# Optimization experiments

Hardware: AMD Instinct MI355X
Metric: run time of the kernel (lower is better)

The kernel has to match this reference:

```python
import jax, jax.numpy as jnp
import numpy as np

N = 30000      # nodes
E = 480000     # edges
F = 128        # num_node_features (== C, required by LSTM-JK stacking of h_list incl. x)
C = 128        # graph_hidden_channels
K = 8          # kernel_size (num gaussians)
D = 2          # pseudo-coordinate dim
L = 4          # nlayers
H = (L * C) // 2   # PyG JK-LSTM hidden size = 256
NHID = 512
NOUT = 256
B = 1024       # number of graphs in batch
EPS = 1e-15


def setup_inputs() -> dict:
    key = jax.random.key(0)
    ks = jax.random.split(key, 24)
    s = 0.05
    inp = {}
    inp['x'] = jax.random.normal(ks[0], (N, F), jnp.float32)
    inp['edge_index'] = jax.random.randint(ks[1], (2, E), 0, N, dtype=jnp.int32)
    inp['edge_attr'] = jax.random.uniform(ks[2], (E, D), jnp.float32)
    inp['batch'] = jnp.sort(jax.random.randint(ks[3], (N,), 0, B, dtype=jnp.int32))
    # GMMConv params per layer (Cin == C for all layers since F == C)
    inp['g'] = jax.random.normal(ks[4], (L, F, K * C), jnp.float32) * s
    inp['root'] = jax.random.normal(ks[5], (L, F, C), jnp.float32) * s
    inp['bias'] = jnp.zeros((L, C), jnp.float32)
    inp['mu'] = jax.random.uniform(ks[6], (L, K, D), jnp.float32)
    inp['sigma'] = jax.random.uniform(ks[7], (L, K, D), jnp.float32) * 0.5 + 0.5
    inp['bn_gamma'] = jnp.ones((L, C), jnp.float32)
    inp['bn_beta'] = jnp.zeros((L, C), jnp.float32)
    # Bidirectional LSTM for JumpingKnowledge: dir 0 = fwd, dir 1 = bwd; gate order i,f,g,o
    inp['w_ih'] = jax.random.normal(ks[8], (2, 4 * H, C), jnp.float32) * s
    inp['w_hh'] = jax.random.normal(ks[9], (2, 4 * H, H), jnp.float32) * s
    inp['b_ih'] = jnp.zeros((2, 4 * H), jnp.float32)
    inp['b_hh'] = jnp.zeros((2, 4 * H), jnp.float32)
    inp['att_w'] = jax.random.normal(ks[10], (2 * H, 1), jnp.float32) * s
    inp['att_b'] = jnp.zeros((1,), jnp.float32)
    inp['p1_w'] = jax.random.normal(ks[11], (C, NHID), jnp.float32) * s
    inp['p1_b'] = jnp.zeros((NHID,), jnp.float32)
    inp['p2_w'] = jax.random.normal(ks[12], (NHID, NOUT), jnp.float32) * s
    inp['p2_b'] = jnp.zeros((NOUT,), jnp.float32)
    inp['ln_g'] = jnp.ones((NOUT,), jnp.float32)
    inp['ln_b'] = jnp.zeros((NOUT,), jnp.float32)
    return inp


def _lstm_dir(xs, w_ih, w_hh, b_ih, b_hh, reverse):
    # xs: [T, N, C] -> hidden states [T, N, H], aligned with input order
    def step(carry, xt):
        h, c = carry
        gates = xt @ w_ih.T + h @ w_hh.T + (b_ih + b_hh)
        i, f, g, o = jnp.split(gates, 4, axis=-1)
        c = jax.nn.sigmoid(f) * c + jax.nn.sigmoid(i) * jnp.tanh(g)
        h = jax.nn.sigmoid(o) * jnp.tanh(c)
        return (h, c), h
    h0 = jnp.zeros((xs.shape[1], w_hh.shape[1]), xs.dtype)
    _, hs = jax.lax.scan(step, (h0, h0), xs, reverse=reverse)
    return hs


def reference(x, edge_index, edge_attr, batch, g, root, bias, mu, sigma,
              bn_gamma, bn_beta, w_ih, w_hh, b_ih, b_hh, att_w, att_b,
              p1_w, p1_b, p2_w, p2_b, ln_g, ln_b):
    src, dst = edge_index[0], edge_index[1]
    deg = jnp.maximum(jax.ops.segment_sum(jnp.ones((E,), x.dtype), dst, num_segments=N), 1.0)[:, None]
    h = x
    h_list = [x]
    for i in range(L):
        # GMMConv: node-level transform then gaussian-weighted message passing (mean aggr)
        xg = (h @ g[i]).reshape(N, K, C)                     # [N, K, C]
        diff = edge_attr[:, None, :] - mu[i][None]           # [E, K, D]
        w = jnp.exp(jnp.sum(-0.5 * diff ** 2 / (EPS + sigma[i][None] ** 2), axis=-1))  # [E, K]
        msg = jnp.zeros((E, C), x.dtype)
        for k in range(K):                                   # small fixed K; avoids [E,K,C] gather
            msg = msg + w[:, k:k + 1] * xg[src, k, :]
        agg = jax.ops.segment_sum(msg, dst, num_segments=N) / deg
        h = agg + h @ root[i] + bias[i]
        # BatchNorm1d (training-mode batch statistics)
        mean = h.mean(0)
        var = h.var(0)
        h = (h - mean) / jnp.sqrt(var + 1e-5) * bn_gamma[i] + bn_beta[i]
        if i < L - 1:
            h = jax.nn.relu(h)
        # dropout is identity in eval mode
        h_list.append(h)
    # JumpingKnowledge, mode='lstm'
    xs = jnp.stack(h_list, axis=0)                           # [L+1, N, C]
    hf = _lstm_dir(xs, w_ih[0], w_hh[0], b_ih[0], b_hh[0], False)
    hb = _lstm_dir(xs, w_ih[1], w_hh[1], b_ih[1], b_hh[1], True)
    seq = jnp.concatenate([hf, hb], axis=-1)                 # [L+1, N, 2H]
    alpha = (seq @ att_w)[..., 0] + att_b[0]                 # [L+1, N]
    alpha = jax.nn.softmax(alpha, axis=0)
    node_rep = jnp.sum(alpha[..., None] * xs, axis=0)        # [N, C]
    # global_mean_pool
    cnt = jnp.maximum(jax.ops.segment_sum(jnp.ones((N,), x.dtype), batch, num_segments=B), 1.0)
    h_graph = jax.ops.segment_sum(node_rep, batch, num_segments=B) / cnt[:, None]
    z = jax.nn.relu(h_graph @ p1_w + p1_b)
    z = z @ p2_w + p2_b
    zm = z.mean(-1, keepdims=True)
    zv = z.var(-1, keepdims=True)
    return (z - zm) / jnp.sqrt(zv + 1e-5) * ln_g + ln_b
```

## Files before the change

kernel.cpp:

```cpp
#include <hip/hip_runtime.h>
#include <hip/hip_bf16.h>
#include <math.h>

#define N_    30000
#define E_    480000
#define C_    128
#define K_    8
#define L_    4
#define H_    256
#define NHID_ 512
#define NOUT_ 256
#define B_    1024
#define SCAN_B 30

typedef __attribute__((ext_vector_type(8))) short short8;
typedef __attribute__((ext_vector_type(4))) float floatx4;
typedef __hip_bfloat16 bf16;

static inline size_t align256(size_t x){ return (x + 255) & ~(size_t)255; }

__device__ __forceinline__ void gload_lds16(const void* g, void* l){
  __builtin_amdgcn_global_load_lds((const __attribute__((address_space(1))) void*)g,
                                   (__attribute__((address_space(3))) void*)l, 16, 0, 0);
}
__device__ __forceinline__ float bf2f(short s){
  union { unsigned u; float f; } x; x.u = ((unsigned)(unsigned short)s) << 16; return x.f;
}

__global__ void hist_k(const int* __restrict__ dst, int* __restrict__ cnt){
  int e = blockIdx.x*256 + threadIdx.x;
  if (e < E_) atomicAdd(&cnt[dst[e]], 1);
}

__global__ void scan1_k(const int* __restrict__ cnt, int* __restrict__ rowptr, int* __restrict__ btot){
  __shared__ int sh[1024];
  int i = blockIdx.x*1024 + (int)threadIdx.x;
  int v = (i < N_) ? cnt[i] : 0;
  sh[threadIdx.x] = v;
  __syncthreads();
  for (int o = 1; o < 1024; o <<= 1){
    int t = (threadIdx.x >= (unsigned)o) ? sh[threadIdx.x - o] : 0;
    __syncthreads();
    sh[threadIdx.x] += t;
    __syncthreads();
  }
  if (i < N_) rowptr[i] = sh[threadIdx.x] - v;
  if (threadIdx.x == 1023) btot[blockIdx.x] = sh[1023];
}
__global__ void scan2_k(const int* __restrict__ btot, int* __restrict__ boff){
  if (threadIdx.x == 0){
    int s = 0;
    for (int b = 0; b < SCAN_B; b++){ boff[b] = s; s += btot[b]; }
    boff[SCAN_B] = s;
  }
}
__global__ void scan3_k(int* __restrict__ rowptr, const int* __restrict__ boff){
  int i = blockIdx.x*1024 + (int)threadIdx.x;
  if (i < N_) rowptr[i] += boff[blockIdx.x];
  if (i == N_-1) rowptr[N_] = boff[SCAN_B];
}

__global__ void degf_k(const int* __restrict__ cnt, float* __restrict__ degf){
  int n = blockIdx.x*256 + threadIdx.x;
  if (n < N_) degf[n] = fmaxf((float)cnt[n], 1.0f);
}

__global__ void scatter_k(const int* __restrict__ src, const int* __restrict__ dst,
                          const int* __restrict__ rowptr, int* __restrict__ fill,
                          int* __restrict__ srcsort, int* __restrict__ edgepos){
  int e = blockIdx.x*256 + threadIdx.x;
  if (e >= E_) return;
  int d = dst[e];
  int pos = rowptr[d] + atomicAdd(&fill[d], 1);
  srcsort[pos] = src[e];
  edgepos[e] = pos;
}

__global__ void cast_k(const float* __restrict__ in, bf16* __restrict__ out, int n){
  int i = blockIdx.x*256 + threadIdx.x;
  if (i < n) out[i] = __float2bfloat16(in[i]);
}
__global__ void tcast_k(const float* __restrict__ in, bf16* __restrict__ out, int R, int Cc){
  const float* ip = in + (size_t)blockIdx.y*R*Cc;
  bf16* op = out + (size_t)blockIdx.y*R*Cc;
  int i = blockIdx.x*256 + threadIdx.x;
  if (i >= R*Cc) return;
  int c = i / R, r = i - c*R;
  op[i] = __float2bfloat16(ip[(size_t)r*Cc + c]);
}
__global__ void gtcast_k(const float* __restrict__ in, bf16* __restrict__ out){
  const float* ip = in + (size_t)blockIdx.y*C_*(K_*C_);
  bf16* op = out + (size_t)blockIdx.y*C_*(K_*C_);
  int i = blockIdx.x*256 + threadIdx.x;
  int co = i >> 10;
  int rem = i & 1023;
  int k = rem >> 7, c = rem & 127;
  op[i] = __float2bfloat16(ip[(size_t)c*(K_*C_) + k*C_ + co]);
}
__global__ void permcast_k(const float* __restrict__ in, bf16* __restrict__ out, int Kdim){
  const float* ip = in + (size_t)blockIdx.y*1024*Kdim;
  bf16* op = out + (size_t)blockIdx.y*1024*Kdim;
  int i = blockIdx.x*256 + threadIdx.x;
  if (i >= 1024*Kdim) return;
  int r = i / Kdim, k = i - r*Kdim;
  int gsel = r >> 8, j = r & 255;
  int rp = ((j >> 5) << 7) + gsel*32 + (j & 31);
  op[(size_t)rp*Kdim + k] = __float2bfloat16(ip[i]);
}
__global__ void permbias_k(const float* __restrict__ bih, const float* __restrict__ bhh,
                           float* __restrict__ bp){
  int i = blockIdx.x*256 + threadIdx.x;
  if (i >= 2048) return;
  int dir = i >> 10, r = i & 1023;
  int gsel = r >> 8, j = r & 255;
  int rp = ((j >> 5) << 7) + gsel*32 + (j & 31);
  bp[dir*1024 + rp] = bih[i] + bhh[i];
}

template<int OUTBF16, int STATS>
__global__ __launch_bounds__(256)
void gemm_bf16_k(const bf16* __restrict__ A1, const bf16* __restrict__ B1, int K1,
                 const bf16* __restrict__ A2, const bf16* __restrict__ B2, int K2,
                 const float* __restrict__ bias1, const float* __restrict__ bias2,
                 void* __restrict__ Cout, int M, int Nn, int relu,
                 float* __restrict__ stats)
{
  __shared__ short As[128*32];
  __shared__ short Bs[128*32];
  __shared__ float colstat[256];
  const int tid  = threadIdx.x;
  const int wave = tid >> 6, lane = tid & 63;
  const int m0 = blockIdx.y*128, n0 = blockIdx.x*128;
  const int wm = (wave >> 1)*64, wn = (wave & 1)*64;
  const int lrow = lane & 15, lk = lane >> 4;
  floatx4 acc[4][4] = {};
  if (STATS) colstat[tid] = 0.f;

  #pragma unroll
  for (int phase = 0; phase < 2; ++phase){
    const bf16* A = phase ? A2 : A1;
    const bf16* B = phase ? B2 : B1;
    const int   K = phase ? K2 : K1;
    if (A == nullptr) continue;
    for (int k0 = 0; k0 < K; k0 += 32){
      #pragma unroll
      for (int i = 0; i < 2; ++i){
        const int chunkbase = i*256 + wave*64;
        const int c   = chunkbase + lane;
        const int row = c >> 2, cc = (c & 3) << 3;
        int ar = m0 + row; if (ar >= M) ar = M - 1;
        gload_lds16(A + (size_t)ar*K + k0 + cc,        As + (size_t)chunkbase*8);
        gload_lds16(B + (size_t)(n0 + row)*K + k0 + cc, Bs + (size_t)chunkbase*8);
      }
      __syncthreads();
      short8 af[4], bfr[4];
      #pragma unroll
      for (int t = 0; t < 4; ++t){
        af[t]  = *(const short8*)&As[((size_t)(wm + t*16 + lrow))*32 + lk*8];
        bfr[t] = *(const short8*)&Bs[((size_t)(wn + t*16 + lrow))*32 + lk*8];
      }
      #pragma unroll
      for (int mt = 0; mt < 4; ++mt)
        #pragma unroll
        for (int nt = 0; nt < 4; ++nt)
          acc[mt][nt] = __builtin_amdgcn_mfma_f32_16x16x32_bf16(af[mt], bfr[nt], acc[mt][nt], 0, 0, 0);
      __syncthreads();
    }
  }

  float* outf = (float*)Cout;
  bf16*  outb = (bf16*)Cout;
  #pragma unroll
  for (int nt = 0; nt < 4; ++nt){
    const int col = n0 + wn + nt*16 + lrow;
    float bv = bias1 ? bias1[col] : 0.f;
    if (bias2) bv += bias2[col];
    float s = 0.f, s2 = 0.f;
    #pragma unroll
    for (int mt = 0; mt < 4; ++mt){
      #pragma unroll
      for (int r = 0; r < 4; ++r){
        const int row = m0 + wm + mt*16 + lk*4 + r;
        if (row >= M) continue;
        float v = acc[mt][nt][r] + bv;
        if (relu) v = fmaxf(v, 0.f);
        if (OUTBF16) outb[(size_t)row*Nn + col] = __float2bfloat16(v);
        else         outf[(size_t)row*Nn + col] = v;
        if (STATS){ s += v; s2 += v*v; }
      }
    }
    if (STATS){
      s  += __shfl_down(s, 16);  s  += __shfl_down(s, 32);
      s2 += __shfl_down(s2, 16); s2 += __shfl_down(s2, 32);
      if (lane < 16){
        atomicAdd(&colstat[wn + nt*16 + lane], s);
        atomicAdd(&colstat[128 + wn + nt*16 + lane], s2);
      }
    }
  }
  if (STATS){
    __syncthreads();
    if (tid < 128){
      atomicAdd(&stats[tid],       colstat[tid]);
      atomicAdd(&stats[128 + tid], colstat[128 + tid]);
    }
  }
}

__global__ __launch_bounds__(256)
void lstm_step_k(const bf16* __restrict__ A1, const bf16* __restrict__ B1,
                 const bf16* __restrict__ A2, const bf16* __restrict__ B2,
                 const float* __restrict__ bp,
                 bf16* __restrict__ hout, float* __restrict__ cst,
                 const float* __restrict__ attw, float* __restrict__ alpha,
                 int M)
{
  __shared__ short As[128*32];
  __shared__ short Bs[128*32];
  __shared__ short gt[128*136];
  const int tid  = threadIdx.x;
  const int wave = tid >> 6, lane = tid & 63;
  const int m0 = blockIdx.y*128, n0 = blockIdx.x*128;
  const int wm = (wave >> 1)*64, wn = (wave & 1)*64;
  const int lrow = lane & 15, lk = lane >> 4;
  floatx4 acc[4][4] = {};

  #pragma unroll
  for (int phase = 0; phase < 2; ++phase){
    const bf16* A = phase ? A2 : A1;
    const bf16* B = phase ? B2 : B1;
    const int   K = phase ? H_ : C_;
    if (A == nullptr) continue;
    for (int k0 = 0; k0 < K; k0 += 32){
      #pragma unroll
      for (int i = 0; i < 2; ++i){
        const int chunkbase = i*256 + wave*64;
        const int c   = chunkbase + lane;
        const int row = c >> 2, cc = (c & 3) << 3;
        int ar = m0 + row; if (ar >= M) ar = M - 1;
        gload_lds16(A + (size_t)ar*K + k0 + cc,        As + (size_t)chunkbase*8);
        gload_lds16(B + (size_t)(n0 + row)*K + k0 + cc, Bs + (size_t)chunkbase*8);
      }
      __syncthreads();
      short8 af[4], bfr[4];
      #pragma unroll
      for (int t = 0; t < 4; ++t){
        af[t]  = *(const short8*)&As[((size_t)(wm + t*16 + lrow))*32 + lk*8];
        bfr[t] = *(const short8*)&Bs[((size_t)(wn + t*16 + lrow))*32 + lk*8];
      }
      #pragma unroll
      for (int mt = 0; mt < 4; ++mt)
        #pragma unroll
        for (int nt = 0; nt < 4; ++nt)
          acc[mt][nt] = __builtin_amdgcn_mfma_f32_16x16x32_bf16(af[mt], bfr[nt], acc[mt][nt], 0, 0, 0);
      __syncthreads();
    }
  }

  #pragma unroll
  for (int nt = 0; nt < 4; ++nt){
    const int col = wn + nt*16 + lrow;
    const float bv = bp[n0 + col];
    #pragma unroll
    for (int mt = 0; mt < 4; ++mt){
      #pragma unroll
      for (int r = 0; r < 4; ++r){
        const int row = wm + mt*16 + lk*4 + r;
        bf16 q = __float2bfloat16(acc[mt][nt][r] + bv);
        gt[row*136 + col] = __builtin_bit_cast(short, q);
      }
    }
  }
  __syncthreads();

  const int row  = tid >> 1, half = tid & 1;
  const int grow = m0 + row;
  float att = 0.f;
  if (grow < M){
    const int chbase = half*16;
    const int jbase  = blockIdx.x*32 + chbase;
    const short8* gp = (const short8*)&gt[row*136 + chbase];
    short8 gv[4][2];
    #pragma unroll
    for (int gsel = 0; gsel < 4; ++gsel){
      gv[gsel][0] = gp[gsel*4];
      gv[gsel][1] = gp[gsel*4 + 1];
    }
    const size_t base = (size_t)grow*H_ + jbase;
    floatx4 cold[4];
    if (A2){
      #pragma unroll
      for (int q = 0; q < 4; ++q) cold[q] = ((const floatx4*)(cst + base))[q];
    } else {
      #pragma unroll
      for (int q = 0; q < 4; ++q) cold[q] = (floatx4){0.f,0.f,0.f,0.f};
    }
    floatx4 cnew[4];
    __hip_bfloat162 hb[8];
    #pragma unroll
    for (int i = 0; i < 16; ++i){
      float gi = bf2f(gv[0][i>>3][i&7]);
      float gf = bf2f(gv[1][i>>3][i&7]);
      float gg = bf2f(gv[2][i>>3][i&7]);
      float go = bf2f(gv[3][i>>3][i&7]);
      float co = cold[i>>2][i&3];
      float ig = 1.f/(1.f + expf(-gi));
      float fg = 1.f/(1.f + expf(-gf));
      float gtv = tanhf(gg);
      float og = 1.f/(1.f + expf(-go));
      float cv = fg*co + ig*gtv;
      float hv = og*tanhf(cv);
      cnew[i>>2][i&3] = cv;
      bf16 hq = __float2bfloat16(hv);
      if (i & 1) hb[i>>1].y = hq; else hb[i>>1].x = hq;
      att = fmaf(hv, attw[jbase + i], att);
    }
    #pragma unroll
    for (int q = 0; q < 4; ++q) ((floatx4*)(cst + base))[q] = cnew[q];
    float4* hp = (float4*)(hout + base);
    hp[0] = *(float4*)&hb[0];
    hp[1] = *(float4*)&hb[4];
  }
  att += __shfl_down(att, 1);
  if (grow < M && half == 0) atomicAdd(&alpha[grow], att);
}

__global__ void compute_w_k(const float* __restrict__ ea, const float* __restrict__ mu,
                            const float* __restrict__ sigma, const int* __restrict__ edgepos,
                            float* __restrict__ wsrt)
{
  int e = blockIdx.x*256 + threadIdx.x;
  if (e >= E_) return;
  float a0 = ea[2*e], a1 = ea[2*e+1];
  int pos = edgepos[e];
  float outv[8];
  #pragma unroll
  for (int k = 0; k < 8; k++){
    float d0 = a0 - mu[2*k],   d1 = a1 - mu[2*k+1];
    float s0 = sigma[2*k],     s1 = sigma[2*k+1];
    float t = -0.5f*(d0*d0/(1e-15f + s0*s0) + d1*d1/(1e-15f + s1*s1));
    outv[k] = expf(t);
  }
  float4* op = (float4*)(wsrt + (size_t)pos*8);
  op[0] = make_float4(outv[0], outv[1], outv[2], outv[3]);
  op[1] = make_float4(outv[4], outv[5], outv[6], outv[7]);
}

__global__ __launch_bounds__(256)
void aggregate_t_k(const bf16* __restrict__ h, const float* __restrict__ wsrt,
                   const int* __restrict__ rowptr, const int* __restrict__ srcsort,
                   const float* __restrict__ degf, bf16* __restrict__ t)
{
  int node = blockIdx.x*4 + (threadIdx.x >> 6);
  int lane = threadIdx.x & 63;
  if (node >= N_) return;
  int p0 = rowptr[node], p1 = rowptr[node+1];
  float ax[8] = {}, ay[8] = {};
  for (int p = p0; p < p1; p++){
    int s = srcsort[p];
    const float4 w03 = *(const float4*)(wsrt + (size_t)p*8);
    const float4 w47 = *(const float4*)(wsrt + (size_t)p*8 + 4);
    const float wk[8] = {w03.x,w03.y,w03.z,w03.w,w47.x,w47.y,w47.z,w47.w};
    float2 v = __bfloat1622float2(((const __hip_bfloat162*)(h + (size_t)s*C_))[lane]);
    #pragma unroll
    for (int k = 0; k < 8; k++){
      ax[k] = fmaf(wk[k], v.x, ax[k]);
      ay[k] = fmaf(wk[k], v.y, ay[k]);
    }
  }
  float inv = 1.0f / degf[node];
  __hip_bfloat162* tp = (__hip_bfloat162*)(t + (size_t)node*(K_*C_));
  #pragma unroll
  for (int k = 0; k < 8; k++){
    __hip_bfloat162 o; o.x = __float2bfloat16(ax[k]*inv); o.y = __float2bfloat16(ay[k]*inv);
    tp[k*64 + lane] = o;
  }
}

__global__ void bn_apply_k(const float* __restrict__ hpre, const float* __restrict__ stats,
                           const float* __restrict__ gamma, const float* __restrict__ beta,
                           bf16* __restrict__ outp, int relu)
{
  int i = blockIdx.x*256 + threadIdx.x;
  if (i >= N_*C_) return;
  int c = i & 127;
  float mean = stats[c] * (1.0f/N_);
  float var  = stats[c+128] * (1.0f/N_) - mean*mean;
  float rstd = rsqrtf(var + 1e-5f);
  float v = (hpre[i] - mean)*rstd*gamma[c] + beta[c];
  if (relu) v = fmaxf(v, 0.f);
  outp[i] = __float2bfloat16(v);
}

__global__ void jk_pool_k(const float* __restrict__ x, const bf16* __restrict__ hlist,
                          const float* __restrict__ alpha, const int* __restrict__ batch,
                          float* __restrict__ hgraph, float* __restrict__ gcnt)
{
  int n = blockIdx.x, c = threadIdx.x;
  float a[5]; float mx = -1e30f;
  #pragma unroll
  for (int t = 0; t < 5; t++){ a[t] = alpha[(size_t)t*N_ + n]; mx = fmaxf(mx, a[t]); }
  float ssum = 0.f;
  #pragma unroll
  for (int t = 0; t < 5; t++){ a[t] = expf(a[t] - mx); ssum += a[t]; }
  float inv = 1.0f/ssum;
  float val = a[0]*inv*x[(size_t)n*C_ + c];
  #pragma unroll
  for (int t = 1; t < 5; t++)
    val = fmaf(a[t]*inv, __bfloat162float(hlist[((size_t)(t-1)*N_ + n)*C_ + c]), val);
  int bg = batch[n];
  atomicAdd(&hgraph[(size_t)bg*C_ + c], val);
  if (c == 0) atomicAdd(&gcnt[bg], 1.0f);
}

__global__ void pool_div_k(const float* __restrict__ hg, const float* __restrict__ gcnt,
                           bf16* __restrict__ hgb){
  int i = blockIdx.x*256 + threadIdx.x;
  if (i < B_*C_) hgb[i] = __float2bfloat16(hg[i] / fmaxf(gcnt[i >> 7], 1.0f));
}

__global__ __launch_bounds__(256)
void layernorm_k(float* __restrict__ z, const float* __restrict__ g, const float* __restrict__ b){
  int row = blockIdx.x, j = threadIdx.x;
  float v = z[(size_t)row*NOUT_ + j];
  float s = v, s2 = v*v;
  #pragma unroll
  for (int o = 32; o; o >>= 1){ s += __shfl_down(s, o); s2 += __shfl_down(s2, o); }
  __shared__ float sh[8];
  int w = j >> 6;
  if ((j & 63) == 0){ sh[w] = s; sh[4+w] = s2; }
  __syncthreads();
  float st  = sh[0] + sh[1] + sh[2] + sh[3];
  float st2 = sh[4] + sh[5] + sh[6] + sh[7];
  float mean = st * (1.0f/NOUT_);
  float var  = st2 * (1.0f/NOUT_) - mean*mean;
  float rstd = rsqrtf(var + 1e-5f);
  z[(size_t)row*NOUT_ + j] = (v - mean)*rstd*g[j] + b[j];
}

extern "C" void kernel_launch(void* const* d_in, const int* in_sizes, int n_in,
                              void* d_out, int out_size, void* d_ws, size_t ws_size,
                              hipStream_t stream)
{
  (void)in_sizes; (void)n_in; (void)out_size; (void)ws_size;
  const float* x     = (const float*)d_in[0];
  const int*   eidx  = (const int*)  d_in[1];
  const float* eattr = (const float*)d_in[2];
  const int*   batch = (const int*)  d_in[3];
  const float* g     = (const float*)d_in[4];
  const float* root  = (const float*)d_in[5];
  const float* bias  = (const float*)d_in[6];
  const float* mu    = (const float*)d_in[7];
  const float* sigma = (const float*)d_in[8];
  const float* bng   = (const float*)d_in[9];
  const float* bnb   = (const float*)d_in[10];
  const float* w_ih  = (const float*)d_in[11];
  const float* w_hh  = (const float*)d_in[12];
  const float* b_ih  = (const float*)d_in[13];
  const float* b_hh  = (const float*)d_in[14];
  const float* attw  = (const float*)d_in[15];
  const float* p1w   = (const float*)d_in[17];
  const float* p1b   = (const float*)d_in[18];
  const float* p2w   = (const float*)d_in[19];
  const float* p2b   = (const float*)d_in[20];
  const float* lng   = (const float*)d_in[21];
  const float* lnb   = (const float*)d_in[22];
  float* outp = (float*)d_out;

  const int* src = eidx;
  const int* dst = eidx + E_;

  size_t off = 0;
  char* wsb = (char*)d_ws;
  auto carve = [&](size_t bytes)->void*{ void* p = wsb + off; off = align256(off + bytes); return p; };
  bf16*  hlist  = (bf16*) carve((size_t)L_*N_*C_*2);
  void*  big    =         carve((size_t)N_*(K_*C_)*2);
  void*  uni    =         carve((size_t)2*N_*H_*2 + (size_t)N_*H_*4 + 256);
  bf16*  xb     = (bf16*) carve((size_t)N_*C_*2);
  float* alpha  = (float*)carve((size_t)(L_+1)*N_*4);
  float* hgraph = (float*)carve((size_t)B_*C_*4);
  bf16*  hgb    = (bf16*) carve((size_t)B_*C_*2);
  float* gcnt   = (float*)carve((size_t)B_*4);
  bf16*  z1b    = (bf16*) carve((size_t)B_*NHID_*2);
  float* bnstats= (float*)carve((size_t)L_*2*C_*4);
  float* degf   = (float*)carve((size_t)N_*4);
  int* cnt      = (int*)  carve((size_t)N_*4);
  int* rowptr   = (int*)  carve((size_t)(N_+1)*4);
  int* fill     = (int*)  carve((size_t)N_*4);
  int* srcsort  = (int*)  carve((size_t)E_*4);
  int* edgepos  = (int*)  carve((size_t)E_*4);
  int* btot     = (int*)  carve((size_t)(SCAN_B+1)*4);
  int* boff     = (int*)  carve((size_t)(SCAN_B+1)*4);
  bf16* gGT   = (bf16*)carve((size_t)L_*C_*(K_*C_)*2);
  bf16* rootT = (bf16*)carve((size_t)L_*C_*C_*2);
  bf16* wihp  = (bf16*)carve((size_t)2*4*H_*C_*2);
  bf16* whhp  = (bf16*)carve((size_t)2*4*H_*H_*2);
  float* bp   = (float*)carve((size_t)2*4*H_*4);
  bf16* p1T   = (bf16*)carve((size_t)NHID_*C_*2);
  bf16* p2T   = (bf16*)carve((size_t)NOUT_*NHID_*2);

  float* wsrt   = (float*)uni;
  float* hpre   = wsrt + (size_t)E_*K_;
  bf16*  hA     = (bf16*)uni;
  bf16*  hB     = hA + (size_t)N_*H_;
  float* cstate = (float*)((char*)uni + (size_t)2*N_*H_*2);
  bf16*  tbuf   = (bf16*)big;

  hipMemsetAsync(cnt,     0, (size_t)N_*4, stream);
  hipMemsetAsync(fill,    0, (size_t)N_*4, stream);
  hipMemsetAsync(bnstats, 0, (size_t)L_*2*C_*4, stream);
  hipMemsetAsync(hgraph,  0, (size_t)B_*C_*4, stream);
  hipMemsetAsync(gcnt,    0, (size_t)B_*4, stream);
  hipMemsetAsync(alpha,   0, (size_t)(L_+1)*N_*4, stream);

  const dim3 blk(256);

  hist_k  <<<(E_+255)/256, 256, 0, stream>>>(dst, cnt);
  scan1_k <<<SCAN_B, 1024, 0, stream>>>(cnt, rowptr, btot);
  scan2_k <<<1, 64, 0, stream>>>(btot, boff);
  scan3_k <<<SCAN_B, 1024, 0, stream>>>(rowptr, boff);
  degf_k  <<<(N_+255)/256, 256, 0, stream>>>(cnt, degf);
  scatter_k<<<(E_+255)/256, 256, 0, stream>>>(src, dst, rowptr, fill, srcsort, edgepos);

  cast_k <<<(N_*C_+255)/256, blk, 0, stream>>>(x, xb, N_*C_);
  gtcast_k<<<dim3((C_*K_*C_)/256, L_), blk, 0, stream>>>(g, gGT);
  tcast_k<<<dim3((C_*C_+255)/256,   L_), blk, 0, stream>>>(root, rootT, C_,   C_);
  permcast_k<<<dim3((1024*C_+255)/256, 2), blk, 0, stream>>>(w_ih, wihp, C_);
  permcast_k<<<dim3((1024*H_+255)/256, 2), blk, 0, stream>>>(w_hh, whhp, H_);
  permbias_k<<<8, blk, 0, stream>>>(b_ih, b_hh, bp);
  tcast_k<<<dim3((C_*NHID_+255)/256, 1), blk, 0, stream>>>(p1w, p1T, C_,    NHID_);
  tcast_k<<<dim3((NHID_*NOUT_+255)/256,1), blk, 0, stream>>>(p2w, p2T, NHID_, NOUT_);

  const int MB = (N_ + 127)/128;

  for (int l = 0; l < L_; l++){
    const bf16* hin = l ? (hlist + (size_t)(l-1)*N_*C_) : xb;
    compute_w_k<<<(E_+255)/256, blk, 0, stream>>>(eattr, mu + (size_t)l*K_*2, sigma + (size_t)l*K_*2, edgepos, wsrt);
    aggregate_t_k<<<N_/4, blk, 0, stream>>>(hin, wsrt, rowptr, srcsort, degf, tbuf);
    gemm_bf16_k<0,1><<<dim3(C_/128, MB), blk, 0, stream>>>(
        tbuf, gGT + (size_t)l*C_*K_*C_, K_*C_, hin, rootT + (size_t)l*C_*C_, C_,
        bias + (size_t)l*C_, nullptr, hpre, N_, C_, 0, bnstats + l*2*C_);
    bn_apply_k<<<(N_*C_+255)/256, blk, 0, stream>>>(hpre, bnstats + l*2*C_, bng + (size_t)l*C_, bnb + (size_t)l*C_,
                                                    hlist + (size_t)l*N_*C_, (l < L_-1) ? 1 : 0);
  }

  for (int dir = 0; dir < 2; dir++){
    const bf16* wih = wihp + (size_t)dir*4*H_*C_;
    const bf16* whh = whhp + (size_t)dir*4*H_*H_;
    const float* bpd = bp + (size_t)dir*4*H_;
    const bf16* hprev = nullptr;
    for (int s = 0; s < 5; s++){
      int t = dir ? 4 - s : s;
      const bf16* xt = t ? (hlist + (size_t)(t-1)*N_*C_) : xb;
      bf16* hnext = (s & 1) ? hB : hA;
      lstm_step_k<<<dim3(8, MB), blk, 0, stream>>>(
          xt, wih, hprev, whh, bpd, hnext, cstate,
          attw + (size_t)dir*H_, alpha + (size_t)t*N_, N_);
      hprev = hnext;
    }
  }

  jk_pool_k<<<N_, 128, 0, stream>>>(x, hlist, alpha, batch, hgraph, gcnt);
  pool_div_k<<<(B_*C_+255)/256, blk, 0, stream>>>(hgraph, gcnt, hgb);

  gemm_bf16_k<1,0><<<dim3(NHID_/128, B_/128), blk, 0, stream>>>(
      hgb, p1T, C_, nullptr, nullptr, 0, p1b, nullptr, z1b, B_, NHID_, 1, nullptr);
  gemm_bf16_k<0,0><<<dim3(NOUT_/128, B_/128), blk, 0, stream>>>(
      z1b, p2T, NHID_, nullptr, nullptr, 0, p2b, nullptr, outp, B_, NOUT_, 0, nullptr);
  layernorm_k<<<B_, 256, 0, stream>>>(outp, lng, lnb);
}
```

Measured before the change: 1.367 ms.

## Compute LSTM gates in registers, store cell state as bf16, use fast math

The weight permutation is changed so each lane's MFMA accumulators already hold the i/f/g/o gates for the same hidden unit. The gate nonlinearities then run directly on registers, and the LDS staging buffer and its extra barrier are removed. Cell state is kept in bf16 instead of fp32, halving its traffic, and sigmoid/tanh use exp plus rcp approximations. Trade-offs: the cell state loses precision across steps, the global stores become strided 2-byte writes, and there are more atomics on alpha.

```diff
diff --git a/kernel.cpp b/kernel.cpp
--- a/kernel.cpp
+++ b/kernel.cpp
@@ -23,9 +23,8 @@
   __builtin_amdgcn_global_load_lds((const __attribute__((address_space(1))) void*)g,
                                    (__attribute__((address_space(3))) void*)l, 16, 0, 0);
 }
-__device__ __forceinline__ float bf2f(short s){
-  union { unsigned u; float f; } x; x.u = ((unsigned)(unsigned short)s) << 16; return x.f;
-}
+__device__ __forceinline__ float sigm_f(float x){ return __builtin_amdgcn_rcpf(1.f + __expf(-x)); }
+__device__ __forceinline__ float tanh_f(float x){ return 1.f - 2.f*__builtin_amdgcn_rcpf(1.f + __expf(2.f*x)); }
 
 __global__ void hist_k(const int* __restrict__ dst, int* __restrict__ cnt){
   int e = blockIdx.x*256 + threadIdx.x;
@@ -103,18 +102,14 @@
   int i = blockIdx.x*256 + threadIdx.x;
   if (i >= 1024*Kdim) return;
   int r = i / Kdim, k = i - r*Kdim;
-  int gsel = r >> 8, j = r & 255;
-  int rp = ((j >> 5) << 7) + gsel*32 + (j & 31);
-  op[(size_t)rp*Kdim + k] = __float2bfloat16(ip[i]);
-}
-__global__ void permbias_k(const float* __restrict__ bih, const float* __restrict__ bhh,
-                           float* __restrict__ bp){
-  int i = blockIdx.x*256 + threadIdx.x;
-  if (i >= 2048) return;
-  int dir = i >> 10, r = i & 1023;
-  int gsel = r >> 8, j = r & 255;
-  int rp = ((j >> 5) << 7) + gsel*32 + (j & 31);
-  bp[dir*1024 + rp] = bih[i] + bhh[i];
+  int gsel = r >> 8, jj = r & 255;
+  int p = ((jj >> 5) << 7) + (((jj >> 4) & 1) << 6) + (gsel << 4) + (jj & 15);
+  op[(size_t)p*Kdim + k] = __float2bfloat16(ip[i]);
+}
+__global__ void biassum_k(const float* __restrict__ bih, const float* __restrict__ bhh,
+                          float* __restrict__ bs){
+  int i = blockIdx.x*256 + threadIdx.x;
+  if (i < 2048) bs[i] = bih[i] + bhh[i];
 }
 
 template<int OUTBF16, int STATS>
@@ -210,14 +205,13 @@
 __global__ __launch_bounds__(256)
 void lstm_step_k(const bf16* __restrict__ A1, const bf16* __restrict__ B1,
                  const bf16* __restrict__ A2, const bf16* __restrict__ B2,
-                 const float* __restrict__ bp,
-                 bf16* __restrict__ hout, float* __restrict__ cst,
+                 const float* __restrict__ bsum,
+                 bf16* __restrict__ hout, bf16* __restrict__ cst,
                  const float* __restrict__ attw, float* __restrict__ alpha,
                  int M)
 {
   __shared__ short As[128*32];
   __shared__ short Bs[128*32];
-  __shared__ short gt[128*136];
   const int tid  = threadIdx.x;
   const int wave = tid >> 6, lane = tid & 63;
   const int m0 = blockIdx.y*128, n0 = blockIdx.x*128;
@@ -257,72 +251,37 @@
     }
   }
 
-  #pragma unroll
-  for (int nt = 0; nt < 4; ++nt){
-    const int col = wn + nt*16 + lrow;
-    const float bv = bp[n0 + col];
+  const int j  = blockIdx.x*32 + (wave & 1)*16 + lrow;
+  const float bi = bsum[0*H_ + j], bff = bsum[1*H_ + j];
+  const float bg = bsum[2*H_ + j], bo  = bsum[3*H_ + j];
+  const float aw = attw[j];
+  #pragma unroll
+  for (int mt = 0; mt < 4; ++mt){
     #pragma unroll
-    for (int mt = 0; mt < 4; ++mt){
-      #pragma unroll
-      for (int r = 0; r < 4; ++r){
-        const int row = wm + mt*16 + lk*4 + r;
-        bf16 q = __float2bfloat16(acc[mt][nt][r] + bv);
-        gt[row*136 + col] = __builtin_bit_cast(short, q);
-      }
-    }
-  }
-  __syncthreads();
-
-  const int row  = tid >> 1, half = tid & 1;
-  const int grow = m0 + row;
-  float att = 0.f;
-  if (grow < M){
-    const int chbase = half*16;
-    const int jbase  = blockIdx.x*32 + chbase;
-    const short8* gp = (const short8*)&gt[row*136 + chbase];
-    short8 gv[4][2];
-    #pragma unroll
-    for (int gsel = 0; gsel < 4; ++gsel){
-      gv[gsel][0] = gp[gsel*4];
-      gv[gsel][1] = gp[gsel*4 + 1];
-    }
-    const size_t base = (size_t)grow*H_ + jbase;
-    floatx4 cold[4];
-    if (A2){
-      #pragma unroll
-      for (int q = 0; q < 4; ++q) cold[q] = ((const floatx4*)(cst + base))[q];
-    } else {
-      #pragma unroll
-      for (int q = 0; q < 4; ++q) cold[q] = (floatx4){0.f,0.f,0.f,0.f};
-    }
-    floatx4 cnew[4];
-    __hip_bfloat162 hb[8];
-    #pragma unroll
-    for (int i = 0; i < 16; ++i){
-      float gi = bf2f(gv[0][i>>3][i&7]);
-      float gf = bf2f(gv[1][i>>3][i&7]);
-      float gg = bf2f(gv[2][i>>3][i&7]);
-      float go = bf2f(gv[3][i>>3][i&7]);
-      float co = cold[i>>2][i&3];
-      float ig = 1.f/(1.f + expf(-gi));
-      float fg = 1.f/(1.f + expf(-gf));
-      float gtv = tanhf(gg);
-      float og = 1.f/(1.f + expf(-go));
-      float cv = fg*co + ig*gtv;
-      float hv = og*tanhf(cv);
-      cnew[i>>2][i&3] = cv;
-      bf16 hq = __float2bfloat16(hv);
-      if (i & 1) hb[i>>1].y = hq; else hb[i>>1].x = hq;
-      att = fmaf(hv, attw[jbase + i], att);
-    }
-    #pragma unroll
-    for (int q = 0; q < 4; ++q) ((floatx4*)(cst + base))[q] = cnew[q];
-    float4* hp = (float4*)(hout + base);
-    hp[0] = *(float4*)&hb[0];
-    hp[1] = *(float4*)&hb[4];
-  }
-  att += __shfl_down(att, 1);
-  if (grow < M && half == 0) atomicAdd(&alpha[grow], att);
+    for (int r = 0; r < 4; ++r){
+      const int row = m0 + wm + mt*16 + lk*4 + r;
+      const bool ok = row < M;
+      const size_t idx = (size_t)row*H_ + j;
+      float co = 0.f;
+      if (A2 && ok) co = __bfloat162float(cst[idx]);
+      float ig = sigm_f(acc[mt][0][r] + bi);
+      float fg = sigm_f(acc[mt][1][r] + bff);
+      float gt = tanh_f(acc[mt][2][r] + bg);
+      float og = sigm_f(acc[mt][3][r] + bo);
+      float cv = fg*co + ig*gt;
+      float hv = og*tanh_f(cv);
+      if (ok){
+        cst[idx]  = __float2bfloat16(cv);
+        hout[idx] = __float2bfloat16(hv);
+      }
+      float att = ok ? hv*aw : 0.f;
+      att += __shfl_xor(att, 1);
+      att += __shfl_xor(att, 2);
+      att += __shfl_xor(att, 4);
+      att += __shfl_xor(att, 8);
+      if (lrow == 0 && ok) atomicAdd(&alpha[row], att);
+    }
+  }
 }
 
 __global__ void compute_w_k(const float* __restrict__ ea, const float* __restrict__ mu,
@@ -475,7 +434,7 @@
   auto carve = [&](size_t bytes)->void*{ void* p = wsb + off; off = align256(off + bytes); return p; };
   bf16*  hlist  = (bf16*) carve((size_t)L_*N_*C_*2);
   void*  big    =         carve((size_t)N_*(K_*C_)*2);
-  void*  uni    =         carve((size_t)2*N_*H_*2 + (size_t)N_*H_*4 + 256);
+  void*  uni    =         carve((size_t)3*N_*H_*2 + 256);
   bf16*  xb     = (bf16*) carve((size_t)N_*C_*2);
   float* alpha  = (float*)carve((size_t)(L_+1)*N_*4);
   float* hgraph = (float*)carve((size_t)B_*C_*4);
@@ -495,7 +454,7 @@
   bf16* rootT = (bf16*)carve((size_t)L_*C_*C_*2);
   bf16* wihp  = (bf16*)carve((size_t)2*4*H_*C_*2);
   bf16* whhp  = (bf16*)carve((size_t)2*4*H_*H_*2);
-  float* bp   = (float*)carve((size_t)2*4*H_*4);
+  float* bsum = (float*)carve((size_t)2*4*H_*4);
   bf16* p1T   = (bf16*)carve((size_t)NHID_*C_*2);
   bf16* p2T   = (bf16*)carve((size_t)NOUT_*NHID_*2);
 
@@ -503,7 +462,7 @@
   float* hpre   = wsrt + (size_t)E_*K_;
   bf16*  hA     = (bf16*)uni;
   bf16*  hB     = hA + (size_t)N_*H_;
-  float* cstate = (float*)((char*)uni + (size_t)2*N_*H_*2);
+  bf16*  cstate = hB + (size_t)N_*H_;
   bf16*  tbuf   = (bf16*)big;
 
   hipMemsetAsync(cnt,     0, (size_t)N_*4, stream);
@@ -527,7 +486,7 @@
   tcast_k<<<dim3((C_*C_+255)/256,   L_), blk, 0, stream>>>(root, rootT, C_,   C_);
   permcast_k<<<dim3((1024*C_+255)/256, 2), blk, 0, stream>>>(w_ih, wihp, C_);
   permcast_k<<<dim3((1024*H_+255)/256, 2), blk, 0, stream>>>(w_hh, whhp, H_);
-  permbias_k<<<8, blk, 0, stream>>>(b_ih, b_hh, bp);
+  biassum_k<<<8, blk, 0, stream>>>(b_ih, b_hh, bsum);
   tcast_k<<<dim3((C_*NHID_+255)/256, 1), blk, 0, stream>>>(p1w, p1T, C_,    NHID_);
   tcast_k<<<dim3((NHID_*NOUT_+255)/256,1), blk, 0, stream>>>(p2w, p2T, NHID_, NOUT_);
 
@@ -547,14 +506,14 @@
   for (int dir = 0; dir < 2; dir++){
     const bf16* wih = wihp + (size_t)dir*4*H_*C_;
     const bf16* whh = whhp + (size_t)dir*4*H_*H_;
-    const float* bpd = bp + (size_t)dir*4*H_;
+    const float* bsd = bsum + (size_t)dir*4*H_;
     const bf16* hprev = nullptr;
     for (int s = 0; s < 5; s++){
       int t = dir ? 4 - s : s;
       const bf16* xt = t ? (hlist + (size_t)(t-1)*N_*C_) : xb;
       bf16* hnext = (s & 1) ? hB : hA;
       lstm_step_k<<<dim3(8, MB), blk, 0, stream>>>(
-          xt, wih, hprev, whh, bpd, hnext, cstate,
+          xt, wih, hprev, whh, bsd, hnext, cstate,
           attw + (size_t)dir*H_, alpha + (size_t)t*N_, N_);
       hprev = hnext;
     }
```

New measurement: 1.324 ms. 3.1% less time.
